# Kernel tuning notes

Hardware: AMD Instinct MI355X
Metric: run time of the kernel (lower is better)

The kernel has to match this reference:

```python
import jax, jax.numpy as jnp
import numpy as np

N = 256   # n_nodes == input_dim (table columns)
B = 1024  # batch size
D = 64    # decoder_dim / encoder_dim


def setup_inputs() -> dict:
    key = jax.random.key(0)
    ks = jax.random.split(key, 10)
    r = lambda k, sh, s=0.05: jax.random.normal(k, sh, dtype=jnp.float32) * s
    return {
        "x": jax.random.normal(ks[0], (B, N), dtype=jnp.float32),
        "eps": jax.random.normal(ks[1], (B, N), dtype=jnp.float32),
        "graph_logits": r(ks[2], (N, N), 0.5),
        "W_enc": r(ks[3], (N, D)),
        "b_enc": jnp.zeros((D,), jnp.float32),
        "W_mu": r(ks[4], (D, N)),
        "b_mu": jnp.zeros((N,), jnp.float32),
        "W_lv": r(ks[5], (D, N)),
        "b_lv": jnp.zeros((N,), jnp.float32),
        "emb_W": r(ks[6], (N, N + 1, D)),   # per-column Linear(input_dim+1 -> decoder_dim)
        "emb_b": jnp.zeros((N, D), jnp.float32),
        "gc1_W": r(ks[7], (D, D // 2)),
        "gc1_b": jnp.zeros((D // 2,), jnp.float32),
        "gc2_W": r(ks[8], (D // 2, 1)),
        "gc2_b": jnp.zeros((1,), jnp.float32),
        "it_num": 10,
    }


def _graph_conv(h, adj, W, b):
    # DGL GraphConv(norm='both', weight, bias) with edge_weight = adj values.
    # Edges go row->col of adj; degrees are unweighted nonzero counts.
    dt = h.dtype
    deg_out = jnp.sum(adj != 0, axis=1).astype(dt)  # out-degree of source node
    deg_in = jnp.sum(adj != 0, axis=0).astype(dt)   # in-degree of destination node
    norm_src = deg_out ** -0.5
    norm_dst = deg_in ** -0.5
    h = h * norm_src[None, :, None]                 # scale source features
    agg = jnp.einsum('bnd,nm->bmd', h, adj)         # sum_i adj[i,j] * h[:, i]
    agg = agg * norm_dst[None, :, None]
    return agg @ W + b


def reference(x, eps, graph_logits, W_enc, b_enc, W_mu, b_mu, W_lv, b_lv,
              emb_W, emb_b, gc1_W, gc1_b, gc2_W, gc2_b, it_num):
    # --- Encoder (MLP-VAE, encoder_l=2 => single Linear+ReLU trunk) ---
    h = jax.nn.relu(x @ W_enc + b_enc)
    mu = h @ W_mu + b_mu
    logvar = h @ W_lv + b_lv
    z = mu + eps * jnp.exp(0.5 * logvar)            # reparameterize, (B, N)
    # --- LearnedGraph ---
    g = jax.nn.sigmoid(graph_logits)
    eye = jnp.eye(N, dtype=g.dtype)
    adj = g * (1.0 - eye) + eye                      # force self-loops to 1
    if it_num > 50:                                  # nn.Threshold(threshold, 0)
        adj = jnp.where(adj > 0.1, adj, 0.0)
    # --- GraphInputProcessorHomo: het encoding + per-column embeddings ---
    b_z = jnp.concatenate(
        [z[:, :, None], jnp.broadcast_to(eye, (z.shape[0], N, N))], axis=-1
    )                                                # (B, N, N+1)
    b_z = jnp.tanh(jnp.einsum('bnf,nfd->bnd', b_z, emb_W) + emb_b[None])  # (B, N, D)
    # --- GraphDecoderHomo ('gcn'): GraphConv(64->32, tanh) -> GraphConv(32->1) ---
    h1 = jnp.tanh(_graph_conv(b_z, adj, gc1_W, gc1_b))
    h2 = _graph_conv(h1, adj, gc2_W, gc2_b)          # (B, N, 1)
    x_hat = h2.reshape(z.shape[0], -1)               # (B, N)
    return x_hat
```

## Files before the change

kernel.cpp:

```cpp
#include <hip/hip_runtime.h>
#include <hip/hip_bf16.h>
#include <math.h>

#define NN 256
#define BB 1024
#define DD 64

typedef short bf16x8 __attribute__((ext_vector_type(8)));
typedef float f32x4 __attribute__((ext_vector_type(4)));

__device__ __forceinline__ float ftanh(float x) {
    float e = __expf(2.0f * x);
    return 1.0f - 2.0f * __builtin_amdgcn_rcpf(e + 1.0f);
}

__device__ __forceinline__ unsigned short f2bf(float v) {
    __hip_bfloat16 h = __float2bfloat16(v);
    return *reinterpret_cast<unsigned short*>(&h);
}

__device__ __forceinline__ float bf2f(unsigned short u) {
    union { unsigned int i; float f; } c;
    c.i = ((unsigned int)u) << 16;
    return c.f;
}

__global__ __launch_bounds__(256) void kA(
    const float* __restrict__ x, const float* __restrict__ eps,
    const float* __restrict__ gl, const float* __restrict__ Wenc,
    const float* __restrict__ benc, const float* __restrict__ Wmu,
    const float* __restrict__ bmu, const float* __restrict__ Wlv,
    const float* __restrict__ blv, const int* __restrict__ itp,
    float* __restrict__ ZT, float* __restrict__ ADJ, float* __restrict__ DEGO)
{
    __shared__ float Hs[4][DD];
    __shared__ int cnt_s[4];
    int t = threadIdx.x;
    int bid = blockIdx.x;

    if (bid < 256) {
        int b0 = bid << 2;
        {
            int d = t & 63, bl = t >> 6;
            const float* xr = x + (b0 + bl) * NN;
            float acc = benc[d];
            for (int n = 0; n < NN; n += 4) {
                float4 xv = *(const float4*)&xr[n];
                acc = fmaf(xv.x, Wenc[(n + 0) * DD + d], acc);
                acc = fmaf(xv.y, Wenc[(n + 1) * DD + d], acc);
                acc = fmaf(xv.z, Wenc[(n + 2) * DD + d], acc);
                acc = fmaf(xv.w, Wenc[(n + 3) * DD + d], acc);
            }
            Hs[bl][d] = fmaxf(acc, 0.0f);
        }
        __syncthreads();
        {
            int n = t;
            float mu[4], lv[4];
            float bm = bmu[n], bl_ = blv[n];
#pragma unroll
            for (int i = 0; i < 4; ++i) { mu[i] = bm; lv[i] = bl_; }
            for (int d = 0; d < DD; ++d) {
                float wm = Wmu[d * NN + n];
                float wl = Wlv[d * NN + n];
#pragma unroll
                for (int i = 0; i < 4; ++i) {
                    float h = Hs[i][d];
                    mu[i] = fmaf(h, wm, mu[i]);
                    lv[i] = fmaf(h, wl, lv[i]);
                }
            }
#pragma unroll
            for (int i = 0; i < 4; ++i) {
                int b = b0 + i;
                ZT[n * BB + b] = fmaf(eps[b * NN + n], expf(0.5f * lv[i]), mu[i]);
            }
        }
    } else {
        int nrow = bid - 256, m = t;
        float v = gl[nrow * NN + m];
        float a = (nrow == m) ? 1.0f : 1.0f / (1.0f + expf(-v));
        if (itp[0] > 50 && !(a > 0.1f)) a = 0.0f;
        ADJ[nrow * NN + m] = a;
        unsigned long long ball = __ballot(a != 0.0f);
        if ((m & 63) == 0) cnt_s[m >> 6] = __popcll(ball);
        __syncthreads();
        if (m == 0) DEGO[nrow] = (float)(cnt_s[0] + cnt_s[1] + cnt_s[2] + cnt_s[3]);
    }
}

__global__ __launch_bounds__(256) void kB(
    const float* __restrict__ ZT, const float* __restrict__ embW,
    const float* __restrict__ embB, const float* __restrict__ g1W,
    const float* __restrict__ ADJ, const float* __restrict__ DEGO,
    float* __restrict__ ADJW, unsigned short* __restrict__ ADJWT,
    unsigned short* __restrict__ P1TT)
{
    __shared__ __align__(16) unsigned char smem[28160];
    int t = threadIdx.x;
    int bid = blockIdx.x;

    if (bid < 256) {
        int m = bid;
        int* cnt_s = (int*)smem;
        float* din_s = (float*)(smem + 16);
        float a = ADJ[t * NN + m];
        unsigned long long ball = __ballot(a != 0.0f);
        if ((t & 63) == 0) cnt_s[t >> 6] = __popcll(ball);
        __syncthreads();
        if (t == 0) din_s[0] = (float)(cnt_s[0] + cnt_s[1] + cnt_s[2] + cnt_s[3]);
        __syncthreads();
        float wv = a * (1.0f / sqrtf(DEGO[t])) * (1.0f / sqrtf(din_s[0]));
        ADJW[t * NN + m] = wv;
        ADJWT[m * NN + t] = f2bf(wv);
    }

    {
        float (*As)[64] = (float(*)[64])(smem);
        float (*Cs)[64] = (float(*)[64])(smem + 1024);
        float (*zsm)[64] = (float(*)[64])(smem + 2048);
        float (*Ws)[68] = (float(*)[68])(smem + 3072);
        unsigned short (*Dst)[32][4] = (unsigned short(*)[32][4])(smem + 11776);
        int w = t >> 6, l = t & 63;
        int lo = l & 15, q = l >> 4;
        int q8 = q << 3;

        for (int i = t; i < 2048; i += 256) {
            int d = i >> 5, k = i & 31;
            Ws[k][d] = g1W[i];
        }
        __syncthreads();

        bf16x8 bwh[2][2], bwl[2][2];
#pragma unroll
        for (int nt = 0; nt < 2; ++nt)
#pragma unroll
            for (int kc = 0; kc < 2; ++kc) {
                float4 w0 = *(const float4*)&Ws[(nt << 4) + lo][(kc << 5) + q8];
                float4 w1 = *(const float4*)&Ws[(nt << 4) + lo][(kc << 5) + q8 + 4];
                float v[8] = {w0.x, w0.y, w0.z, w0.w, w1.x, w1.y, w1.z, w1.w};
                bf16x8 h, lq;
#pragma unroll
                for (int j = 0; j < 8; ++j) {
                    unsigned short hb = f2bf(v[j]);
                    h[j] = (short)hb;
                    lq[j] = (short)f2bf(v[j] - bf2f(hb));
                }
                bwh[nt][kc] = h;
                bwl[nt][kc] = lq;
            }

        for (int it = 0; it < 2; ++it) {
            int tile = (bid << 1) | it;
            int nb = tile & 63, bb2 = tile >> 6;
            int n0 = nb << 2, b0 = bb2 << 6;
            __syncthreads();
            {
                int ni = t >> 6, d = t & 63;
                size_t eb = (size_t)(n0 + ni) * (257 * 64);
                As[ni][d] = embW[eb + d];
                Cs[ni][d] = embW[eb + ((size_t)(n0 + ni + 1) << 6) + d]
                          + embB[((n0 + ni) << 6) + d];
                zsm[ni][d] = ZT[(size_t)(n0 + ni) * BB + b0 + d];
            }
            __syncthreads();
#pragma unroll
            for (int ni = 0; ni < 4; ++ni) {
                float zv = zsm[ni][(w << 4) + lo];
                f32x4 acc0 = (f32x4)0.0f, acc1 = (f32x4)0.0f;
#pragma unroll
                for (int kc = 0; kc < 2; ++kc) {
                    float4 a0 = *(const float4*)&As[ni][(kc << 5) + q8];
                    float4 a1 = *(const float4*)&As[ni][(kc << 5) + q8 + 4];
                    float4 c0 = *(const float4*)&Cs[ni][(kc << 5) + q8];
                    float4 c1 = *(const float4*)&Cs[ni][(kc << 5) + q8 + 4];
                    float e[8];
                    e[0] = ftanh(fmaf(zv, a0.x, c0.x));
                    e[1] = ftanh(fmaf(zv, a0.y, c0.y));
                    e[2] = ftanh(fmaf(zv, a0.z, c0.z));
                    e[3] = ftanh(fmaf(zv, a0.w, c0.w));
                    e[4] = ftanh(fmaf(zv, a1.x, c1.x));
                    e[5] = ftanh(fmaf(zv, a1.y, c1.y));
                    e[6] = ftanh(fmaf(zv, a1.z, c1.z));
                    e[7] = ftanh(fmaf(zv, a1.w, c1.w));
                    bf16x8 ehi, elo;
#pragma unroll
                    for (int j = 0; j < 8; ++j) {
                        unsigned short hb = f2bf(e[j]);
                        ehi[j] = (short)hb;
                        elo[j] = (short)f2bf(e[j] - bf2f(hb));
                    }
                    acc0 = __builtin_amdgcn_mfma_f32_16x16x32_bf16(ehi, bwh[0][kc], acc0, 0, 0, 0);
                    acc0 = __builtin_amdgcn_mfma_f32_16x16x32_bf16(elo, bwh[0][kc], acc0, 0, 0, 0);
                    acc0 = __builtin_amdgcn_mfma_f32_16x16x32_bf16(ehi, bwl[0][kc], acc0, 0, 0, 0);
                    acc1 = __builtin_amdgcn_mfma_f32_16x16x32_bf16(ehi, bwh[1][kc], acc1, 0, 0, 0);
                    acc1 = __builtin_amdgcn_mfma_f32_16x16x32_bf16(elo, bwh[1][kc], acc1, 0, 0, 0);
                    acc1 = __builtin_amdgcn_mfma_f32_16x16x32_bf16(ehi, bwl[1][kc], acc1, 0, 0, 0);
                }
                int bl = (w << 4) + (q << 2);
#pragma unroll
                for (int r = 0; r < 4; ++r) {
                    Dst[bl + r][lo][ni]      = f2bf(acc0[r]);
                    Dst[bl + r][16 + lo][ni] = f2bf(acc1[r]);
                }
            }
            __syncthreads();
            const uint2* dsp = (const uint2*)&Dst[0][0][0];
            size_t obase = ((size_t)b0 * 32) * NN + n0;
#pragma unroll
            for (int i = 0; i < 8; ++i) {
                int p = (i << 8) + t;
                uint2 v = dsp[p];
                *(uint2*)&P1TT[obase + (size_t)p * NN] = v;
            }
        }
    }
}

__global__ __launch_bounds__(256) void kC(
    const unsigned short* __restrict__ adjwt, const unsigned short* __restrict__ p1tt,
    const float* __restrict__ g1b, const float* __restrict__ g2w,
    float* __restrict__ Q)
{
    int t = threadIdx.x;
    int w = t >> 6, l = t & 63;
    int c = l & 15, q = l >> 4;
    int jt = blockIdx.x >> 1, mh = blockIdx.x & 1;
    int j0 = jt << 6;
    int mbase = (mh << 7) + (w << 5);

    f32x4 acc[2][4];
#pragma unroll
    for (int i = 0; i < 2; ++i)
#pragma unroll
        for (int j = 0; j < 4; ++j) acc[i][j] = (f32x4)0.0f;

    const unsigned short* ap[2];
    const unsigned short* bp[4];
#pragma unroll
    for (int mi = 0; mi < 2; ++mi)
        ap[mi] = adjwt + (size_t)(mbase + (mi << 4) + c) * NN + (q << 3);
#pragma unroll
    for (int ji = 0; ji < 4; ++ji)
        bp[ji] = p1tt + (size_t)(j0 + (ji << 4) + c) * NN + (q << 3);

#pragma unroll 2
    for (int n0 = 0; n0 < NN; n0 += 32) {
        bf16x8 af[2], bf[4];
#pragma unroll
        for (int mi = 0; mi < 2; ++mi) af[mi] = *(const bf16x8*)(ap[mi] + n0);
#pragma unroll
        for (int ji = 0; ji < 4; ++ji) bf[ji] = *(const bf16x8*)(bp[ji] + n0);
#pragma unroll
        for (int mi = 0; mi < 2; ++mi)
#pragma unroll
            for (int ji = 0; ji < 4; ++ji)
                acc[mi][ji] = __builtin_amdgcn_mfma_f32_16x16x32_bf16(
                    af[mi], bf[ji], acc[mi][ji], 0, 0, 0);
    }

    float b1v0 = g1b[c],      g2v0 = g2w[c];
    float b1v1 = g1b[16 + c], g2v1 = g2w[16 + c];
    int bb0 = jt << 1;
#pragma unroll
    for (int mi = 0; mi < 2; ++mi) {
#pragma unroll
        for (int bb = 0; bb < 2; ++bb) {
            float red[4];
#pragma unroll
            for (int r = 0; r < 4; ++r) {
                float s = ftanh(acc[mi][(bb << 1) + 0][r] + b1v0) * g2v0
                        + ftanh(acc[mi][(bb << 1) + 1][r] + b1v1) * g2v1;
                s += __shfl_xor(s, 1);
                s += __shfl_xor(s, 2);
                s += __shfl_xor(s, 4);
                s += __shfl_xor(s, 8);
                red[r] = s;
            }
            float* qp = &Q[(size_t)(bb0 + bb) * NN + mbase + (mi << 4) + (q << 2)];
            if (c == 0) qp[0] = red[0];
            if (c == 1) qp[1] = red[1];
            if (c == 2) qp[2] = red[2];
            if (c == 3) qp[3] = red[3];
        }
    }
}

__global__ __launch_bounds__(256) void kD(
    const float* __restrict__ Q, const float* __restrict__ adjw,
    const float* __restrict__ g2b, float* __restrict__ xh)
{
    __shared__ float At[32][33];
    __shared__ float Bt[32][33];
    int t = threadIdx.x;
    int tx = t & 15, ty = t >> 4;
    int mt = blockIdx.x & 7, bt = blockIdx.x >> 3;
    int m0 = mt << 5, b0 = bt << 5;
    float acc[2][2] = {{0.0f, 0.0f}, {0.0f, 0.0f}};

    for (int kb = 0; kb < NN; kb += 32) {
        for (int i = t; i < 1024; i += 256) {
            int r = i >> 5, cc = i & 31;
            At[r][cc] = Q[(b0 + r) * NN + kb + cc];
            Bt[r][cc] = adjw[(kb + r) * NN + m0 + cc];
        }
        __syncthreads();
#pragma unroll 8
        for (int kk = 0; kk < 32; ++kk) {
            float bv0 = Bt[kk][tx << 1], bv1 = Bt[kk][(tx << 1) + 1];
            float a0 = At[ty << 1][kk], a1 = At[(ty << 1) + 1][kk];
            acc[0][0] = fmaf(a0, bv0, acc[0][0]);
            acc[0][1] = fmaf(a0, bv1, acc[0][1]);
            acc[1][0] = fmaf(a1, bv0, acc[1][0]);
            acc[1][1] = fmaf(a1, bv1, acc[1][1]);
        }
        __syncthreads();
    }
    float bias = g2b[0];
#pragma unroll
    for (int i = 0; i < 2; ++i) {
        float2 v = make_float2(acc[i][0] + bias, acc[i][1] + bias);
        *(float2*)&xh[(b0 + (ty << 1) + i) * NN + m0 + (tx << 1)] = v;
    }
}

extern "C" void kernel_launch(void* const* d_in, const int* in_sizes, int n_in,
                              void* d_out, int out_size, void* d_ws, size_t ws_size,
                              hipStream_t stream) {
    const float* x    = (const float*)d_in[0];
    const float* eps  = (const float*)d_in[1];
    const float* gl   = (const float*)d_in[2];
    const float* Wenc = (const float*)d_in[3];
    const float* benc = (const float*)d_in[4];
    const float* Wmu  = (const float*)d_in[5];
    const float* bmu  = (const float*)d_in[6];
    const float* Wlv  = (const float*)d_in[7];
    const float* blv  = (const float*)d_in[8];
    const float* embW = (const float*)d_in[9];
    const float* embB = (const float*)d_in[10];
    const float* g1W  = (const float*)d_in[11];
    const float* g1b  = (const float*)d_in[12];
    const float* g2W  = (const float*)d_in[13];
    const float* g2b  = (const float*)d_in[14];
    const int*   itp  = (const int*)d_in[15];

    float* ws   = (float*)d_ws;
    float* ZT   = ws + 65536;
    float* ADJ  = ws + 327680;
    float* DEGO = ws + 393216;
    float* ADJW = ws + 393472;
    unsigned short* ADJWT = (unsigned short*)(ws + 459008);
    unsigned short* P1TT  = (unsigned short*)(ws + 491776);
    float* Qb   = ws + 4686080;
    float* xh   = (float*)d_out;

    kA<<<512,  256, 0, stream>>>(x, eps, gl, Wenc, benc, Wmu, bmu, Wlv, blv,
                                 itp, ZT, ADJ, DEGO);
    kB<<<512,  256, 0, stream>>>(ZT, embW, embB, g1W, ADJ, DEGO, ADJW, ADJWT, P1TT);
    kC<<<1024, 256, 0, stream>>>(ADJWT, P1TT, g1b, g2W, Qb);
    kD<<<256,  256, 0, stream>>>(Qb, ADJW, g2b, xh);
}
```

Baseline: 178.4 us.

## Fuse second graph-conv aggregation into MFMA kernel via shared-memory Q

Merges kC and kD into one kernel. Each block now covers both m-halves for its two batch rows and writes the reduced Q vector to shared memory instead of global. It then does the final adjacency matvec directly, so the Q round-trip and one launch go away. The cost is half as many blocks for the MFMA stage, and every block re-reads the full 256x256 fp32 adjacency for a serial 256-step matvec.

```diff
diff --git a/kernel.cpp b/kernel.cpp
--- a/kernel.cpp
+++ b/kernel.cpp
@@ -217,110 +217,93 @@
     }
 }
 
-__global__ __launch_bounds__(256) void kC(
+__global__ __launch_bounds__(256) void kCD(
     const unsigned short* __restrict__ adjwt, const unsigned short* __restrict__ p1tt,
     const float* __restrict__ g1b, const float* __restrict__ g2w,
-    float* __restrict__ Q)
+    const float* __restrict__ adjw, const float* __restrict__ g2b,
+    float* __restrict__ xh)
 {
+    __shared__ float Qs[2][NN];
     int t = threadIdx.x;
     int w = t >> 6, l = t & 63;
     int c = l & 15, q = l >> 4;
-    int jt = blockIdx.x >> 1, mh = blockIdx.x & 1;
+    int jt = blockIdx.x;
     int j0 = jt << 6;
-    int mbase = (mh << 7) + (w << 5);
-
-    f32x4 acc[2][4];
-#pragma unroll
-    for (int i = 0; i < 2; ++i)
-#pragma unroll
-        for (int j = 0; j < 4; ++j) acc[i][j] = (f32x4)0.0f;
-
-    const unsigned short* ap[2];
+    int bb0 = jt << 1;
+
+    float b1v0 = g1b[c],      g2v0 = g2w[c];
+    float b1v1 = g1b[16 + c], g2v1 = g2w[16 + c];
+
     const unsigned short* bp[4];
-#pragma unroll
-    for (int mi = 0; mi < 2; ++mi)
-        ap[mi] = adjwt + (size_t)(mbase + (mi << 4) + c) * NN + (q << 3);
 #pragma unroll
     for (int ji = 0; ji < 4; ++ji)
         bp[ji] = p1tt + (size_t)(j0 + (ji << 4) + c) * NN + (q << 3);
 
+#pragma unroll
+    for (int mh = 0; mh < 2; ++mh) {
+        int mbase = (mh << 7) + (w << 5);
+        f32x4 acc[2][4];
+#pragma unroll
+        for (int i = 0; i < 2; ++i)
+#pragma unroll
+            for (int j = 0; j < 4; ++j) acc[i][j] = (f32x4)0.0f;
+
+        const unsigned short* ap[2];
+#pragma unroll
+        for (int mi = 0; mi < 2; ++mi)
+            ap[mi] = adjwt + (size_t)(mbase + (mi << 4) + c) * NN + (q << 3);
+
 #pragma unroll 2
-    for (int n0 = 0; n0 < NN; n0 += 32) {
-        bf16x8 af[2], bf[4];
-#pragma unroll
-        for (int mi = 0; mi < 2; ++mi) af[mi] = *(const bf16x8*)(ap[mi] + n0);
-#pragma unroll
-        for (int ji = 0; ji < 4; ++ji) bf[ji] = *(const bf16x8*)(bp[ji] + n0);
-#pragma unroll
-        for (int mi = 0; mi < 2; ++mi)
-#pragma unroll
-            for (int ji = 0; ji < 4; ++ji)
-                acc[mi][ji] = __builtin_amdgcn_mfma_f32_16x16x32_bf16(
-                    af[mi], bf[ji], acc[mi][ji], 0, 0, 0);
-    }
-
-    float b1v0 = g1b[c],      g2v0 = g2w[c];
-    float b1v1 = g1b[16 + c], g2v1 = g2w[16 + c];
-    int bb0 = jt << 1;
-#pragma unroll
-    for (int mi = 0; mi < 2; ++mi) {
-#pragma unroll
-        for (int bb = 0; bb < 2; ++bb) {
-            float red[4];
-#pragma unroll
-            for (int r = 0; r < 4; ++r) {
-                float s = ftanh(acc[mi][(bb << 1) + 0][r] + b1v0) * g2v0
-                        + ftanh(acc[mi][(bb << 1) + 1][r] + b1v1) * g2v1;
-                s += __shfl_xor(s, 1);
-                s += __shfl_xor(s, 2);
-                s += __shfl_xor(s, 4);
-                s += __shfl_xor(s, 8);
-                red[r] = s;
-            }
-            float* qp = &Q[(size_t)(bb0 + bb) * NN + mbase + (mi << 4) + (q << 2)];
-            if (c == 0) qp[0] = red[0];
-            if (c == 1) qp[1] = red[1];
-            if (c == 2) qp[2] = red[2];
-            if (c == 3) qp[3] = red[3];
-        }
-    }
-}
-
-__global__ __launch_bounds__(256) void kD(
-    const float* __restrict__ Q, const float* __restrict__ adjw,
-    const float* __restrict__ g2b, float* __restrict__ xh)
-{
-    __shared__ float At[32][33];
-    __shared__ float Bt[32][33];
-    int t = threadIdx.x;
-    int tx = t & 15, ty = t >> 4;
-    int mt = blockIdx.x & 7, bt = blockIdx.x >> 3;
-    int m0 = mt << 5, b0 = bt << 5;
-    float acc[2][2] = {{0.0f, 0.0f}, {0.0f, 0.0f}};
-
-    for (int kb = 0; kb < NN; kb += 32) {
-        for (int i = t; i < 1024; i += 256) {
-            int r = i >> 5, cc = i & 31;
-            At[r][cc] = Q[(b0 + r) * NN + kb + cc];
-            Bt[r][cc] = adjw[(kb + r) * NN + m0 + cc];
-        }
-        __syncthreads();
-#pragma unroll 8
-        for (int kk = 0; kk < 32; ++kk) {
-            float bv0 = Bt[kk][tx << 1], bv1 = Bt[kk][(tx << 1) + 1];
-            float a0 = At[ty << 1][kk], a1 = At[(ty << 1) + 1][kk];
-            acc[0][0] = fmaf(a0, bv0, acc[0][0]);
-            acc[0][1] = fmaf(a0, bv1, acc[0][1]);
-            acc[1][0] = fmaf(a1, bv0, acc[1][0]);
-            acc[1][1] = fmaf(a1, bv1, acc[1][1]);
-        }
-        __syncthreads();
-    }
-    float bias = g2b[0];
-#pragma unroll
-    for (int i = 0; i < 2; ++i) {
-        float2 v = make_float2(acc[i][0] + bias, acc[i][1] + bias);
-        *(float2*)&xh[(b0 + (ty << 1) + i) * NN + m0 + (tx << 1)] = v;
+        for (int n0 = 0; n0 < NN; n0 += 32) {
+            bf16x8 af[2], bf[4];
+#pragma unroll
+            for (int mi = 0; mi < 2; ++mi) af[mi] = *(const bf16x8*)(ap[mi] + n0);
+#pragma unroll
+            for (int ji = 0; ji < 4; ++ji) bf[ji] = *(const bf16x8*)(bp[ji] + n0);
+#pragma unroll
+            for (int mi = 0; mi < 2; ++mi)
+#pragma unroll
+                for (int ji = 0; ji < 4; ++ji)
+                    acc[mi][ji] = __builtin_amdgcn_mfma_f32_16x16x32_bf16(
+                        af[mi], bf[ji], acc[mi][ji], 0, 0, 0);
+        }
+
+#pragma unroll
+        for (int mi = 0; mi < 2; ++mi) {
+#pragma unroll
+            for (int bb = 0; bb < 2; ++bb) {
+                float red[4];
+#pragma unroll
+                for (int r = 0; r < 4; ++r) {
+                    float s = ftanh(acc[mi][(bb << 1) + 0][r] + b1v0) * g2v0
+                            + ftanh(acc[mi][(bb << 1) + 1][r] + b1v1) * g2v1;
+                    s += __shfl_xor(s, 1);
+                    s += __shfl_xor(s, 2);
+                    s += __shfl_xor(s, 4);
+                    s += __shfl_xor(s, 8);
+                    red[r] = s;
+                }
+                float* qp = &Qs[bb][mbase + (mi << 4) + (q << 2)];
+                if (c == 0) qp[0] = red[0];
+                if (c == 1) qp[1] = red[1];
+                if (c == 2) qp[2] = red[2];
+                if (c == 3) qp[3] = red[3];
+            }
+        }
+    }
+    __syncthreads();
+
+    {
+        int mp = t;
+        float a0 = 0.0f, a1 = 0.0f;
+        for (int k = 0; k < NN; ++k) {
+            float wv = adjw[k * NN + mp];
+            a0 = fmaf(Qs[0][k], wv, a0);
+            a1 = fmaf(Qs[1][k], wv, a1);
+        }
+        float bias = g2b[0];
+        xh[(size_t)(bb0 + 0) * NN + mp] = a0 + bias;
+        xh[(size_t)(bb0 + 1) * NN + mp] = a1 + bias;
     }
 }
 
@@ -351,12 +334,10 @@
     float* ADJW = ws + 393472;
     unsigned short* ADJWT = (unsigned short*)(ws + 459008);
     unsigned short* P1TT  = (unsigned short*)(ws + 491776);
-    float* Qb   = ws + 4686080;
     float* xh   = (float*)d_out;
 
-    kA<<<512,  256, 0, stream>>>(x, eps, gl, Wenc, benc, Wmu, bmu, Wlv, blv,
+    kA <<<512, 256, 0, stream>>>(x, eps, gl, Wenc, benc, Wmu, bmu, Wlv, blv,
                                  itp, ZT, ADJ, DEGO);
-    kB<<<512,  256, 0, stream>>>(ZT, embW, embB, g1W, ADJ, DEGO, ADJW, ADJWT, P1TT);
-    kC<<<1024, 256, 0, stream>>>(ADJWT, P1TT, g1b, g2W, Qb);
-    kD<<<256,  256, 0, stream>>>(Qb, ADJW, g2b, xh);
-}
+    kB <<<512, 256, 0, stream>>>(ZT, embW, embB, g1W, ADJ, DEGO, ADJW, ADJWT, P1TT);
+    kCD<<<512, 256, 0, stream>>>(ADJWT, P1TT, g1b, g2W, ADJW, g2b, xh);
+}
```

Result: faster. 170.6 us (-4.4%).
